# Kernel optimization log

Hardware: AMD Instinct MI355X
Metric: run time of the kernel (lower is better)

Reference implementation:

```python
import jax, jax.numpy as jnp
import numpy as np
import math

EPS = 1e-9
NORM = 1.0 / math.sqrt(20.0)  # num_neighbours=20 default


def _mixing(x1, x2, B, W, b):
    # nn.Bilinear (no bias): x_bi[n,k] = sum_ij x1[n,i] B[k,i,j] x2[n,j]
    x_bi = jnp.einsum('ni,kij->nkj', x1, B)
    x_bi = jnp.einsum('nkj,nj->nk', x_bi, x2)
    x = jnp.concatenate([x1, x2, x_bi], axis=-1)
    return x @ W.T + b


def _rowstd(x):
    # torch.std default: unbiased (ddof=1)
    return jnp.std(x, axis=1, ddof=1, keepdims=True)


def setup_inputs() -> dict:
    key = jax.random.key(0)
    N, E = 100000, 2000000
    DN, DE, DA_N, DA_E = 32, 32, 3, 1
    ks = jax.random.split(key, 24)

    def nrm(k, shape, fan_in):
        return jax.random.normal(k, shape, dtype=jnp.float32) / np.sqrt(fan_in)

    inp = {
        'xn': jax.random.normal(ks[0], (N, DN), dtype=jnp.float32),
        'xn_attr': jax.random.normal(ks[1], (N, DA_N), dtype=jnp.float32),
        'xe_attr': jax.random.normal(ks[2], (E, DA_E), dtype=jnp.float32),
        'xe_src': jax.random.randint(ks[3], (E,), 0, N),
        'xe_dst': jax.random.randint(ks[4], (E,), 0, N),
        # fc1: Linear(1, xe_dim); fc2: Linear(1, xn_dim)
        'W_fc1': nrm(ks[5], (DE, 1), 1), 'b_fc1': jnp.zeros((DE,), jnp.float32),
        'W_fc2': nrm(ks[6], (DN, 1), 1), 'b_fc2': jnp.zeros((DN,), jnp.float32),
        # mix_xn: Mixing(DN, DA_N, DN)
        'B_mix_xn': nrm(ks[7], (DN, DN, DA_N), DN * DA_N),
        'W_mix_xn': nrm(ks[8], (DN, 2 * DN + DA_N), 2 * DN + DA_N),
        'b_mix_xn': jnp.zeros((DN,), jnp.float32),
        # nodes_to_edges.mix: Mixing(DN, DN, DN)
        'B_n2e': nrm(ks[9], (DN, DN, DN), DN * DN),
        'W_n2e': nrm(ks[10], (DN, 3 * DN), 3 * DN),
        'b_n2e': jnp.zeros((DN,), jnp.float32),
        # mix_xe: Mixing(DE, DA_E, DE)
        'B_mix_xe': nrm(ks[11], (DE, DE, DA_E), DE * DA_E),
        'W_mix_xe': nrm(ks[12], (DE, 2 * DE + DA_E), 2 * DE + DA_E),
        'b_mix_xe': jnp.zeros((DE,), jnp.float32),
        # edges_to_nodes.mix: Mixing(DE, DE, DE)
        'B_e2n': nrm(ks[13], (DE, DE, DE), DE * DE),
        'W_e2n': nrm(ks[14], (DE, 3 * DE), 3 * DE),
        'b_e2n': jnp.zeros((DE,), jnp.float32),
    }
    return inp


def reference(xn, xn_attr, xe_attr, xe_src, xe_dst,
              W_fc1, b_fc1, W_fc2, b_fc2,
              B_mix_xn, W_mix_xn, b_mix_xn,
              B_n2e, W_n2e, b_n2e,
              B_mix_xe, W_mix_xe, b_mix_xe,
              B_e2n, W_e2n, b_e2n):
    n_nodes = xn.shape[0]
    # node mixing + per-row std norm
    xn = _mixing(xn, xn_attr, B_mix_xn, W_mix_xn, b_mix_xn)
    xn = xn / (_rowstd(xn) + EPS)
    # fc1 weight: [E, xe_dim]
    w1 = jax.nn.silu(xe_attr @ W_fc1.T + b_fc1)
    # NodesToEdges: gather -> grad/ave -> mixing
    xg, xd = xn[xe_src], xn[xe_dst]
    xe = _mixing(w1 * (xg - xd), w1 * (xg + xd) * 0.5, B_n2e, W_n2e, b_n2e)
    xe = _mixing(xe, xe_attr, B_mix_xe, W_mix_xe, b_mix_xe)
    xe = xe / (_rowstd(xe) + EPS)
    # fc2 weight: [E, xn_dim]
    w2 = jax.nn.silu(xe_attr @ W_fc2.T + b_fc2)
    # EdgesToNodes: scatter-add over dst/src, diff/sum, mixing
    wxe = w2 * xe
    xn1 = jax.ops.segment_sum(wxe, xe_dst, num_segments=n_nodes) * NORM
    xn2 = jax.ops.segment_sum(wxe, xe_src, num_segments=n_nodes) * NORM
    xn = _mixing(xn1 - xn2, xn1 + xn2, B_e2n, W_e2n, b_e2n)
    xn = jax.nn.silu(xn)
    xn = xn / (_rowstd(xn) + EPS)
    return xn
```

## Files before the change

### kernel.cpp

```cpp
#include <hip/hip_runtime.h>
#include <hip/hip_bf16.h>

#define N_NODES 100000
#define N_EDGES 2000000
#define EPS 1e-9f
#define NORMC 0.22360679774997896f

#define BKSZ   256
#define NBK1   391
#define NBK    782
#define NSB    256
#define CE     7813
#define NITEMS 4000000

typedef short s8 __attribute__((ext_vector_type(8)));
typedef float f4 __attribute__((ext_vector_type(4)));

__device__ __forceinline__ float silu_f(float x) {
    return x / (1.0f + __expf(-x));
}

__device__ __forceinline__ ushort f2bfu(float f) {
    union { __hip_bfloat16 b; ushort u; } cv;
    cv.b = __float2bfloat16(f);
    return cv.u;
}

__device__ __forceinline__ uint pkbf(float lo, float hi) {
    float2 t; t.x = lo; t.y = hi;
    union { __hip_bfloat162 b; uint u; } cv;
    cv.b = __float22bfloat162_rn(t);
    return cv.u;
}


__device__ float mext(const float* __restrict__ W, const float* __restrict__ B,
                      const float* __restrict__ bias, int n, int i, int j) {
    if (i < 32 && j < 32) {
        float r = 0.f;
        #pragma unroll
        for (int m = 0; m < 32; ++m) r += W[n*96 + 64 + m] * B[m*1024 + i*32 + j];
        return r;
    }
    if (i < 32) return W[n*96 + i];
    if (j < 32) return W[n*96 + 32 + j];
    return bias[n];
}

__global__ void prep_kernel(const float* __restrict__ W_n2e, const float* __restrict__ B_n2e,
                            const float* __restrict__ b_n2e,
                            const float* __restrict__ W_e2n, const float* __restrict__ B_e2n,
                            const float* __restrict__ b_e2n,
                            const float* __restrict__ W_mix_xn, const float* __restrict__ B_mix_xn,
                            const float* __restrict__ b_mix_xn,
                            const float* __restrict__ W_mix_xe, const float* __restrict__ B_mix_xe,
                            const float* __restrict__ b_mix_xe,
                            ushort* __restrict__ MF, ushort* __restrict__ MG,
                            float* __restrict__ BpN, float* __restrict__ WxE,
                            float* __restrict__ CtE) {
    int t = blockIdx.x * blockDim.x + threadIdx.x;
    if (t < 69632) {
        int u = (t < 34816) ? t : t - 34816;
        int tt = u & 7, lane = (u >> 3) & 63, rest = u >> 9;
        int nt = rest & 1, kk = rest >> 1;
        int n = nt*16 + (lane & 15);
        int kl = ((lane >> 4) & 3) * 8 + tt;
        int i, j;
        if (kk < 33) { i = kk; j = kl; } else { i = kl; j = 32; }
        if (t < 34816) MF[u] = f2bfu(mext(W_n2e, B_n2e, b_n2e, n, i, j));
        else           MG[u] = f2bfu(mext(W_e2n, B_e2n, b_e2n, n, i, j));
    } else if (t < 73856) {
        int u = t - 69632;
        int k = u & 31, ij = u >> 5;
        int i = ij >> 2, j = ij & 3;
        float r;
        if (i < 32 && j < 3) {
            r = 0.f;
            #pragma unroll
            for (int m = 0; m < 32; ++m) r += W_mix_xn[k*67 + 35 + m] * B_mix_xn[m*96 + i*3 + j];
        } else if (i < 32 && j == 3) {
            r = W_mix_xn[k*67 + i];
        } else if (i == 32 && j < 3) {
            r = W_mix_xn[k*67 + 32 + j];
        } else {
            r = b_mix_xn[k];
        }
        BpN[ij*32 + k] = r;
    } else if (t < 74912) {
        int u = t - 73856;
        int k = u & 31, i = u >> 5;
        WxE[i*32 + k] = (i < 32) ? W_mix_xe[k*65 + i] : b_mix_xe[k];
    } else if (t < 75968) {
        int u = t - 74912;
        int k = u & 31, i = u >> 5;
        float r;
        if (i < 32) {
            r = 0.f;
            #pragma unroll
            for (int m = 0; m < 32; ++m) r += W_mix_xe[k*65 + 33 + m] * B_mix_xe[m*32 + i];
        } else {
            r = W_mix_xe[k*65 + 32];
        }
        CtE[i*32 + k] = r;
    }
}

__global__ void zero_kernel(float4* __restrict__ p, int n4) {
    int i = blockIdx.x * blockDim.x + threadIdx.x;
    int stride = gridDim.x * blockDim.x;
    float4 z = {0.f, 0.f, 0.f, 0.f};
    for (; i < n4; i += stride) p[i] = z;
}

__global__ __launch_bounds__(256) void node_kernel(
    const float* __restrict__ xn, const float* __restrict__ xn_attr,
    const float* __restrict__ BpN, float* __restrict__ xn_norm) {
    int n = blockIdx.x * 256 + threadIdx.x;
    if (n >= N_NODES) return;
    float x[33];
    const float4* xr = (const float4*)(xn + (size_t)n * 32);
    #pragma unroll
    for (int q = 0; q < 8; ++q) {
        float4 v = xr[q];
        x[q*4+0] = v.x; x[q*4+1] = v.y; x[q*4+2] = v.z; x[q*4+3] = v.w;
    }
    x[32] = 1.f;
    float at[4];
    at[0] = xn_attr[n*3]; at[1] = xn_attr[n*3+1]; at[2] = xn_attr[n*3+2]; at[3] = 1.f;

    float acc[32];
    #pragma unroll
    for (int k = 0; k < 32; ++k) acc[k] = 0.f;
    #pragma unroll
    for (int i = 0; i < 33; ++i) {
        #pragma unroll
        for (int j = 0; j < 4; ++j) {
            float s = x[i] * at[j];
            const float* bp = BpN + (i*4 + j) * 32;
            #pragma unroll
            for (int k = 0; k < 32; ++k) acc[k] = fmaf(bp[k], s, acc[k]);
        }
    }
    float mean = 0.f;
    #pragma unroll
    for (int k = 0; k < 32; ++k) mean += acc[k];
    mean *= (1.0f / 32.0f);
    float var = 0.f;
    #pragma unroll
    for (int k = 0; k < 32; ++k) { float d = acc[k] - mean; var += d * d; }
    var *= (1.0f / 31.0f);
    float inv = 1.0f / (sqrtf(var) + EPS);
    float4* out = (float4*)(xn_norm + (size_t)n * 32);
    #pragma unroll
    for (int q = 0; q < 8; ++q) {
        float4 v;
        v.x = acc[q*4+0]*inv; v.y = acc[q*4+1]*inv; v.z = acc[q*4+2]*inv; v.w = acc[q*4+3]*inv;
        out[q] = v;
    }
}


__global__ __launch_bounds__(256) void count_kernel(
    const int* __restrict__ xe_src, const int* __restrict__ xe_dst,
    int* __restrict__ cntg) {
    __shared__ int cnt[NBK];
    int tid = threadIdx.x, b = blockIdx.x;
    for (int k = tid; k < NBK; k += 256) cnt[k] = 0;
    __syncthreads();
    int e0 = b * CE;
    for (int i = tid; i < CE; i += 256) {
        int e = e0 + i;
        if (e < N_EDGES) {
            atomicAdd(&cnt[xe_dst[e] >> 8], 1);
            atomicAdd(&cnt[NBK1 + (xe_src[e] >> 8)], 1);
        }
    }
    __syncthreads();
    for (int k = tid; k < NBK; k += 256) cntg[k * NSB + b] = cnt[k];
}

#define SCAN_TOT (NBK * NSB)

__global__ __launch_bounds__(1024) void scan_kernel(
    const int* __restrict__ cntg, int* __restrict__ scang) {
    __shared__ int part[1024];
    int t = threadIdx.x;
    const int CHUNK = 196;
    int base = t * CHUNK;
    int s = 0;
    for (int i = 0; i < CHUNK; ++i) {
        int idx = base + i;
        if (idx < SCAN_TOT) s += cntg[idx];
    }
    part[t] = s;
    __syncthreads();
    for (int off = 1; off < 1024; off <<= 1) {
        int v = part[t];
        int add = (t >= off) ? part[t - off] : 0;
        __syncthreads();
        part[t] = v + add;
        __syncthreads();
    }
    int run = (t == 0) ? 0 : part[t - 1];
    for (int i = 0; i < CHUNK; ++i) {
        int idx = base + i;
        if (idx < SCAN_TOT) {
            int c = cntg[idx];
            scang[idx] = run;
            run += c;
        }
    }
}

__global__ __launch_bounds__(256) void scatter_kernel(
    const int* __restrict__ xe_src, const int* __restrict__ xe_dst,
    const int* __restrict__ scang, int* __restrict__ bucketed) {
    __shared__ int cur[NBK];
    int tid = threadIdx.x, b = blockIdx.x;
    for (int k = tid; k < NBK; k += 256) cur[k] = scang[k * NSB + b];
    __syncthreads();
    int e0 = b * CE;
    for (int i = tid; i < CE; i += 256) {
        int e = e0 + i;
        if (e < N_EDGES) {
            int d = xe_dst[e];
            int p = atomicAdd(&cur[d >> 8], 1);
            bucketed[p] = e | ((d & 255) << 21);
            int s_ = xe_src[e];
            p = atomicAdd(&cur[NBK1 + (s_ >> 8)], 1);
            bucketed[p] = e | ((s_ & 255) << 21);
        }
    }
}

__global__ __launch_bounds__(256) void gather_kernel(
    const ushort* __restrict__ wxe, const int* __restrict__ bucketed,
    const int* __restrict__ scang, float* __restrict__ sd0) {
    __shared__ float accs[BKSZ * 33];
    int tid = threadIdx.x, bk = blockIdx.x;
    for (int i = tid; i < BKSZ * 33; i += 256) accs[i] = 0.f;
    __syncthreads();
    int start = scang[bk * NSB];
    int end = (bk == NBK - 1) ? NITEMS : scang[(bk + 1) * NSB];
    int q = tid >> 2, g = tid & 3;
    uint4 z4; z4.x = 0u; z4.y = 0u; z4.z = 0u; z4.w = 0u;

    int i0 = start + q;
    int p0 = (i0 < end) ? bucketed[i0] : 0;
    int p1 = (i0 + 64 < end) ? bucketed[i0 + 64] : 0;
    uint4 r0 = (i0 < end)
             ? *(const uint4*)(wxe + (size_t)(p0 & 0x1FFFFF) * 32 + g * 8) : z4;

    for (int i = i0; i < end; i += 64) {
        int pn = (i + 128 < end) ? bucketed[i + 128] : 0;
        uint4 r1 = (i + 64 < end)
                 ? *(const uint4*)(wxe + (size_t)(p1 & 0x1FFFFF) * 32 + g * 8) : z4;
        int ln = (p0 >> 21) & 255;
        float* ap = &accs[ln * 33 + g * 8];
        uint uu[4] = {r0.x, r0.y, r0.z, r0.w};
        #pragma unroll
        for (int c = 0; c < 4; ++c) {
            uint u = uu[c];
            atomicAdd(&ap[c*2],     __uint_as_float((u & 0xFFFFu) << 16));
            atomicAdd(&ap[c*2 + 1], __uint_as_float(u & 0xFFFF0000u));
        }
        p0 = p1; p1 = pn; r0 = r1;
    }
    __syncthreads();
    int side = (bk < NBK1) ? 0 : 1;
    int nb = side ? bk - NBK1 : bk;
    float* out = sd0 + (size_t)side * 3211264 + (size_t)nb * BKSZ * 32;
    for (int i = tid; i < BKSZ * 32; i += 256) {
        int node = i >> 5, k = i & 31;
        out[i] = accs[node * 33 + k];
    }
}


__device__ __forceinline__ void gemm33(const ushort* __restrict__ sM,
                                       float* __restrict__ a_f,
                                       const ushort* __restrict__ ab,
                                       const float* __restrict__ biasv, int tid) {
    int lane = tid & 63, wv = tid >> 6;
    int m = lane & 15, h = lane >> 4;
    int base = wv * 64;
    float bfv[4][8];
    s8 araw[4];
    #pragma unroll
    for (int g = 0; g < 4; ++g) {
        const ushort* rp = &ab[(size_t)(base + g*16 + m) * 72];
        union { s8 v; ushort s[8]; } braw;
        braw.v = *(const s8*)&rp[h*8];
        #pragma unroll
        for (int t = 0; t < 8; ++t) {
            union { uint u; float f; } cv; cv.u = ((uint)braw.s[t]) << 16;
            bfv[g][t] = cv.f;
        }
        araw[g] = *(const s8*)&rp[32 + h*8];
    }
    f4 c[4][2];
    #pragma unroll
    for (int g = 0; g < 4; ++g) {
        c[g][0] = (f4){0.f, 0.f, 0.f, 0.f};
        c[g][1] = (f4){0.f, 0.f, 0.f, 0.f};
    }
    const s8* M8 = (const s8*)sM;
    #pragma unroll
    for (int kk = 0; kk < 33; ++kk) {
        s8 mf0 = M8[(kk*2 + 0)*64 + lane];
        s8 mf1 = M8[(kk*2 + 1)*64 + lane];
        #pragma unroll
        for (int g = 0; g < 4; ++g) {
            float as = a_f[(size_t)(base + g*16 + m) * 33 + kk];
            union { s8 v; uint u[4]; } af;
            #pragma unroll
            for (int t = 0; t < 4; ++t) af.u[t] = pkbf(as * bfv[g][2*t], as * bfv[g][2*t+1]);
            c[g][0] = __builtin_amdgcn_mfma_f32_16x16x32_bf16(af.v, mf0, c[g][0], 0, 0, 0);
            c[g][1] = __builtin_amdgcn_mfma_f32_16x16x32_bf16(af.v, mf1, c[g][1], 0, 0, 0);
        }
    }
    {
        s8 mf0 = M8[66*64 + lane];
        s8 mf1 = M8[67*64 + lane];
        #pragma unroll
        for (int g = 0; g < 4; ++g) {
            c[g][0] = __builtin_amdgcn_mfma_f32_16x16x32_bf16(araw[g], mf0, c[g][0], 0, 0, 0);
            c[g][1] = __builtin_amdgcn_mfma_f32_16x16x32_bf16(araw[g], mf1, c[g][1], 0, 0, 0);
        }
    }
    float b0 = biasv[m], b1 = biasv[16 + m];
    #pragma unroll
    for (int g = 0; g < 4; ++g) {
        int rowb = base + g*16 + h*4;
        #pragma unroll
        for (int r = 0; r < 4; ++r) {
            a_f[(size_t)(rowb + r) * 33 + m]      = c[g][0][r] + b0;
            a_f[(size_t)(rowb + r) * 33 + 16 + m] = c[g][1][r] + b1;
        }
    }
}

#define TILES_E 7813

template<bool STORE>
__global__ __launch_bounds__(256, 1) void edge_kernel(
    const float* __restrict__ xn_norm, const float* __restrict__ xe_attr,
    const int* __restrict__ xe_src, const int* __restrict__ xe_dst,
    const float* __restrict__ W_fc1, const float* __restrict__ b_fc1,
    const float* __restrict__ W_fc2, const float* __restrict__ b_fc2,
    const ushort* __restrict__ MF, const float* __restrict__ biasE,
    const float* __restrict__ WxE, const float* __restrict__ CtE,
    float* __restrict__ acc1, float* __restrict__ acc2,
    ushort* __restrict__ wxe) {
    __shared__ __align__(16) ushort sM[34816];
    __shared__ __align__(16) float  a_f[256 * 33];
    __shared__ __align__(16) ushort ab[256 * 72];
    int tid = threadIdx.x;
    {
        const float4* s4p = (const float4*)MF;
        float4* d4p = (float4*)sM;
        #pragma unroll
        for (int i = 0; i < 17; ++i) d4p[tid + i*256] = s4p[tid + i*256];
    }
    uint* ab32 = (uint*)ab;

    int t = blockIdx.x;
    float attrP = 0.f; int srcP = 0, dstP = 0; bool okP = false;
    float4 gP[8], dP[8];
    {
        int e = t*256 + tid;
        okP = e < N_EDGES;
        int ec = okP ? e : 0;
        attrP = xe_attr[ec]; srcP = xe_src[ec]; dstP = xe_dst[ec];
        const float4* gp = (const float4*)(xn_norm + (size_t)srcP * 32);
        const float4* dp = (const float4*)(xn_norm + (size_t)dstP * 32);
        #pragma unroll
        for (int q = 0; q < 8; ++q) { gP[q] = gp[q]; dP[q] = dp[q]; }
    }

    for (; t < TILES_E; t += 256) {
        float attr = attrP; int csrc = srcP, cdst = dstP; bool okC = okP;
        float vs = okC ? 1.f : 0.f;
        #pragma unroll
        for (int q = 0; q < 8; ++q) {
            float4 g = gP[q], d = dP[q];
            float gg[4] = {g.x, g.y, g.z, g.w};
            float dd[4] = {d.x, d.y, d.z, d.w};
            #pragma unroll
            for (int p = 0; p < 2; ++p) {
                int k = q*4 + p*2;
                float w0 = silu_f(attr * W_fc1[k]   + b_fc1[k])   * vs;
                float w1 = silu_f(attr * W_fc1[k+1] + b_fc1[k+1]) * vs;
                float av0 = w0 * (gg[2*p]   - dd[2*p]);
                float av1 = w1 * (gg[2*p+1] - dd[2*p+1]);
                float bv0 = w0 * (gg[2*p]   + dd[2*p])   * 0.5f;
                float bv1 = w1 * (gg[2*p+1] + dd[2*p+1]) * 0.5f;
                a_f[tid*33 + k]   = av0;
                a_f[tid*33 + k+1] = av1;
                ab32[tid*36 + (k>>1)]      = pkbf(bv0, bv1);
                ab32[tid*36 + 16 + (k>>1)] = pkbf(av0, av1);
            }
        }
        a_f[tid*33 + 32] = 1.f;

        int tn = t + 256;
        if (tn < TILES_E) {
            int e = tn*256 + tid;
            okP = e < N_EDGES;
            int ec = okP ? e : 0;
            attrP = xe_attr[ec]; srcP = xe_src[ec]; dstP = xe_dst[ec];
            const float4* gp = (const float4*)(xn_norm + (size_t)srcP * 32);
            const float4* dp = (const float4*)(xn_norm + (size_t)dstP * 32);
            #pragma unroll
            for (int q = 0; q < 8; ++q) { gP[q] = gp[q]; dP[q] = dp[q]; }
        }
        __syncthreads();

        gemm33(sM, a_f, ab, biasE, tid);
        __syncthreads();

        float2 y2[16];
        #pragma unroll
        for (int k2 = 0; k2 < 16; ++k2) y2[k2] = make_float2(0.f, 0.f);
        for (int i = 0; i < 33; ++i) {
            float xi = a_f[tid*33 + i];
            const float2* wx2 = (const float2*)(WxE + i * 32);
            const float2* ct2 = (const float2*)(CtE + i * 32);
            #pragma unroll
            for (int k2 = 0; k2 < 16; ++k2) {
                float2 w = wx2[k2], ctv = ct2[k2];
                float lx = fmaf(attr, ctv.x, w.x);
                float ly = fmaf(attr, ctv.y, w.y);
                y2[k2].x = fmaf(lx, xi, y2[k2].x);
                y2[k2].y = fmaf(ly, xi, y2[k2].y);
            }
        }
        float mean = 0.f;
        #pragma unroll
        for (int k2 = 0; k2 < 16; ++k2) mean += y2[k2].x + y2[k2].y;
        mean *= (1.0f / 32.0f);
        float var = 0.f;
        #pragma unroll
        for (int k2 = 0; k2 < 16; ++k2) {
            float dx = y2[k2].x - mean, dy = y2[k2].y - mean;
            var += dx*dx + dy*dy;
        }
        var *= (1.0f / 31.0f);
        float inv = 1.0f / (sqrtf(var) + EPS);

        if (okC) {
            if (STORE) {
                uint pkv[16];
                #pragma unroll
                for (int k2 = 0; k2 < 16; ++k2) {
                    float w20 = silu_f(attr * W_fc2[2*k2]   + b_fc2[2*k2]);
                    float w21 = silu_f(attr * W_fc2[2*k2+1] + b_fc2[2*k2+1]);
                    pkv[k2] = pkbf(w20 * y2[k2].x * inv, w21 * y2[k2].y * inv);
                }
                uint4* wp = (uint4*)(wxe + (size_t)(t*256 + tid) * 32);
                #pragma unroll
                for (int q = 0; q < 4; ++q) {
                    uint4 v; v.x = pkv[q*4]; v.y = pkv[q*4+1]; v.z = pkv[q*4+2]; v.w = pkv[q*4+3];
                    wp[q] = v;
                }
            } else {
                float* p1 = acc1 + (size_t)cdst * 32;
                float* p2 = acc2 + (size_t)csrc * 32;
                #pragma unroll
                for (int k = 0; k < 32; ++k) {
                    float yk = (k & 1) ? y2[k>>1].y : y2[k>>1].x;
                    float w2 = silu_f(attr * W_fc2[k] + b_fc2[k]);
                    float v = w2 * yk * inv;
                    unsafeAtomicAdd(p1 + k, v);
                    unsafeAtomicAdd(p2 + k, v);
                }
            }
        }
    }
}

#define TILES_F 391

__global__ __launch_bounds__(256, 1) void final_kernel(
    const float* __restrict__ acc1, const float* __restrict__ acc2,
    const ushort* __restrict__ MG, const float* __restrict__ biasG,
    float* __restrict__ out) {
    __shared__ __align__(16) ushort sM[34816];
    __shared__ __align__(16) float  a_f[256 * 33];
    __shared__ __align__(16) ushort ab[256 * 72];
    int tid = threadIdx.x;
    {
        const float4* s4p = (const float4*)MG;
        float4* d4p = (float4*)sM;
        #pragma unroll
        for (int i = 0; i < 17; ++i) d4p[tid + i*256] = s4p[tid + i*256];
    }
    uint* ab32 = (uint*)ab;

    for (int t = blockIdx.x; t < TILES_F; t += 256) {
        int n = t*256 + tid;
        bool ok = n < N_NODES;
        int nn = ok ? n : 0;
        float vs = ok ? 1.f : 0.f;
        const float4* p1 = (const float4*)(acc1 + (size_t)nn * 32);
        const float4* p2 = (const float4*)(acc2 + (size_t)nn * 32);
        #pragma unroll
        for (int q = 0; q < 8; ++q) {
            float4 u1 = p1[q], u2 = p2[q];
            float a1[4] = {u1.x, u1.y, u1.z, u1.w};
            float a2[4] = {u2.x, u2.y, u2.z, u2.w};
            #pragma unroll
            for (int p = 0; p < 2; ++p) {
                int k = q*4 + p*2;
                float dv0 = (a1[2*p]   - a2[2*p])   * NORMC * vs;
                float dv1 = (a1[2*p+1] - a2[2*p+1]) * NORMC * vs;
                float sv0 = (a1[2*p]   + a2[2*p])   * NORMC * vs;
                float sv1 = (a1[2*p+1] + a2[2*p+1]) * NORMC * vs;
                a_f[tid*33 + k]   = dv0;
                a_f[tid*33 + k+1] = dv1;
                ab32[tid*36 + (k>>1)]      = pkbf(sv0, sv1);
                ab32[tid*36 + 16 + (k>>1)] = pkbf(dv0, dv1);
            }
        }
        a_f[tid*33 + 32] = 1.f;
        __syncthreads();

        gemm33(sM, a_f, ab, biasG, tid);
        __syncthreads();

        if (ok) {
            float z[32];
            float mean = 0.f;
            #pragma unroll
            for (int k = 0; k < 32; ++k) { z[k] = silu_f(a_f[tid*33 + k]); mean += z[k]; }
            mean *= (1.0f / 32.0f);
            float var = 0.f;
            #pragma unroll
            for (int k = 0; k < 32; ++k) { float d = z[k] - mean; var += d * d; }
            var *= (1.0f / 31.0f);
            float inv = 1.0f / (sqrtf(var) + EPS);
            float4* op = (float4*)(out + (size_t)n * 32);
            #pragma unroll
            for (int q = 0; q < 8; ++q) {
                float4 v;
                v.x = z[q*4+0]*inv; v.y = z[q*4+1]*inv; v.z = z[q*4+2]*inv; v.w = z[q*4+3]*inv;
                op[q] = v;
            }
        }
    }
}

extern "C" void kernel_launch(void* const* d_in, const int* in_sizes, int n_in,
                              void* d_out, int out_size, void* d_ws, size_t ws_size,
                              hipStream_t stream) {
    const float* xn       = (const float*)d_in[0];
    const float* xn_attr  = (const float*)d_in[1];
    const float* xe_attr  = (const float*)d_in[2];
    const int*   xe_src   = (const int*)d_in[3];
    const int*   xe_dst   = (const int*)d_in[4];
    const float* W_fc1    = (const float*)d_in[5];
    const float* b_fc1    = (const float*)d_in[6];
    const float* W_fc2    = (const float*)d_in[7];
    const float* b_fc2    = (const float*)d_in[8];
    const float* B_mix_xn = (const float*)d_in[9];
    const float* W_mix_xn = (const float*)d_in[10];
    const float* b_mix_xn = (const float*)d_in[11];
    const float* B_n2e    = (const float*)d_in[12];
    const float* W_n2e    = (const float*)d_in[13];
    const float* b_n2e    = (const float*)d_in[14];
    const float* B_mix_xe = (const float*)d_in[15];
    const float* W_mix_xe = (const float*)d_in[16];
    const float* b_mix_xe = (const float*)d_in[17];
    const float* B_e2n    = (const float*)d_in[18];
    const float* W_e2n    = (const float*)d_in[19];
    const float* b_e2n    = (const float*)d_in[20];

    float* ws = (float*)d_ws;
    const size_t MAIN_BYTES = 46065088ULL * 4ULL;
    bool big = ws_size >= MAIN_BYTES;

    if (big) {
        float*  xn_norm = ws;
        float*  sd0     = ws + 3200000;
        float*  sd1     = ws + 6411264;
        ushort* MF      = (ushort*)(ws + 9622528);
        ushort* MG      = MF + 34816;
        float*  BpN     = ws + 9657344;
        float*  WxE     = ws + 9661568;
        float*  CtE     = ws + 9662624;
        ushort* wxe     = (ushort*)(ws + 9663680);
        int*    bucketed= (int*)(ws + 41663680);
        int*    cntg    = (int*)(ws + 45663680);
        int*    scang   = (int*)(ws + 45864384);

        prep_kernel<<<297, 256, 0, stream>>>(W_n2e, B_n2e, b_n2e, W_e2n, B_e2n, b_e2n,
                                             W_mix_xn, B_mix_xn, b_mix_xn,
                                             W_mix_xe, B_mix_xe, b_mix_xe,
                                             MF, MG, BpN, WxE, CtE);
        node_kernel<<<391, 256, 0, stream>>>(xn, xn_attr, BpN, xn_norm);
        count_kernel<<<NSB, 256, 0, stream>>>(xe_src, xe_dst, cntg);
        scan_kernel<<<1, 1024, 0, stream>>>(cntg, scang);
        scatter_kernel<<<NSB, 256, 0, stream>>>(xe_src, xe_dst, scang, bucketed);
        edge_kernel<true><<<256, 256, 0, stream>>>(xn_norm, xe_attr, xe_src, xe_dst,
                                                   W_fc1, b_fc1, W_fc2, b_fc2,
                                                   MF, b_n2e, WxE, CtE,
                                                   nullptr, nullptr, wxe);
        gather_kernel<<<NBK, 256, 0, stream>>>(wxe, bucketed, scang, sd0);
        final_kernel<<<391, 256, 0, stream>>>(sd0, sd1, MG, b_e2n, (float*)d_out);
    } else {
        float*  xn_norm = ws;
        float*  acc1    = ws + 3200000;
        float*  acc2    = ws + 6400000;
        ushort* MF      = (ushort*)(ws + 9600000);
        ushort* MG      = MF + 34816;
        float*  BpN     = ws + 9600000 + 34816;
        float*  WxE     = BpN + 4224;
        float*  CtE     = WxE + 1056;

        prep_kernel<<<297, 256, 0, stream>>>(W_n2e, B_n2e, b_n2e, W_e2n, B_e2n, b_e2n,
                                             W_mix_xn, B_mix_xn, b_mix_xn,
                                             W_mix_xe, B_mix_xe, b_mix_xe,
                                             MF, MG, BpN, WxE, CtE);
        zero_kernel<<<2048, 256, 0, stream>>>((float4*)acc1, 1600000);
        node_kernel<<<391, 256, 0, stream>>>(xn, xn_attr, BpN, xn_norm);
        edge_kernel<false><<<256, 256, 0, stream>>>(xn_norm, xe_attr, xe_src, xe_dst,
                                                    W_fc1, b_fc1, W_fc2, b_fc2,
                                                    MF, b_n2e, WxE, CtE,
                                                    acc1, acc2, nullptr);
        final_kernel<<<391, 256, 0, stream>>>(acc1, acc2, MG, b_e2n, (float*)d_out);
    }
}
```

Before: 2.013 ms.

## Store edge outputs in src-bucket order and split gather into src/dst passes

The edge kernel now writes each edge's weighted message directly to its position in the source-sorted order, using a position array built during scatter. The src-side gather then reads contiguously with a byte lane index, and the dst-side gather indexes through a packed (position, lane) array. The gemm staging buffer is shrunk by recomputing the bf16 copy of the first operand from the float tile instead of storing it twice. This trades scattered reads in the gather for scattered writes in the edge kernel and adds an extra per-edge index load.

```diff
diff --git a/kernel.cpp b/kernel.cpp
--- a/kernel.cpp
+++ b/kernel.cpp
@@ -11,10 +11,13 @@
 #define NBK    782
 #define NSB    256
 #define CE     7813
-#define NITEMS 4000000
+#define SCAN_TOT (NBK * NSB)
+#define TILES_E 7813
+#define TILES_F 391
 
 typedef short s8 __attribute__((ext_vector_type(8)));
 typedef float f4 __attribute__((ext_vector_type(4)));
+typedef uint  u4 __attribute__((ext_vector_type(4)));
 
 __device__ __forceinline__ float silu_f(float x) {
     return x / (1.0f + __expf(-x));
@@ -179,10 +182,7 @@
     for (int k = tid; k < NBK; k += 256) cntg[k * NSB + b] = cnt[k];
 }
 
-#define SCAN_TOT (NBK * NSB)
-
-__global__ __launch_bounds__(1024) void scan_kernel(
-    const int* __restrict__ cntg, int* __restrict__ scang) {
+__global__ __launch_bounds__(1024) void scan_kernel(int* __restrict__ cntg) {
     __shared__ int part[1024];
     int t = threadIdx.x;
     const int CHUNK = 196;
@@ -206,7 +206,7 @@
         int idx = base + i;
         if (idx < SCAN_TOT) {
             int c = cntg[idx];
-            scang[idx] = run;
+            cntg[idx] = run;
             run += c;
         }
     }
@@ -214,7 +214,8 @@
 
 __global__ __launch_bounds__(256) void scatter_kernel(
     const int* __restrict__ xe_src, const int* __restrict__ xe_dst,
-    const int* __restrict__ scang, int* __restrict__ bucketed) {
+    const int* __restrict__ scang, int* __restrict__ poss,
+    unsigned char* __restrict__ srcln, int* __restrict__ bucketed_dst) {
     __shared__ int cur[NBK];
     int tid = threadIdx.x, b = blockIdx.x;
     for (int k = tid; k < NBK; k += 256) cur[k] = scang[k * NSB + b];
@@ -223,39 +224,77 @@
     for (int i = tid; i < CE; i += 256) {
         int e = e0 + i;
         if (e < N_EDGES) {
+            int s_ = xe_src[e];
+            int p2 = atomicAdd(&cur[NBK1 + (s_ >> 8)], 1) - N_EDGES;
+            poss[e] = p2;
+            srcln[p2] = (unsigned char)(s_ & 255);
             int d = xe_dst[e];
-            int p = atomicAdd(&cur[d >> 8], 1);
-            bucketed[p] = e | ((d & 255) << 21);
-            int s_ = xe_src[e];
-            p = atomicAdd(&cur[NBK1 + (s_ >> 8)], 1);
-            bucketed[p] = e | ((s_ & 255) << 21);
-        }
-    }
-}
-
-__global__ __launch_bounds__(256) void gather_kernel(
-    const ushort* __restrict__ wxe, const int* __restrict__ bucketed,
+            int pd = atomicAdd(&cur[d >> 8], 1);
+            bucketed_dst[pd] = (p2 << 8) | (d & 255);
+        }
+    }
+}
+
+__global__ __launch_bounds__(256) void gather_src(
+    const ushort* __restrict__ wxe2, const unsigned char* __restrict__ srcln,
+    const int* __restrict__ scang, float* __restrict__ sd1) {
+    __shared__ float accs[BKSZ * 33];
+    int tid = threadIdx.x, bk = blockIdx.x;
+    for (int i = tid; i < BKSZ * 33; i += 256) accs[i] = 0.f;
+    __syncthreads();
+    int start = scang[(NBK1 + bk) * NSB] - N_EDGES;
+    int end = (bk == NBK1 - 1) ? N_EDGES : scang[(NBK1 + bk + 1) * NSB] - N_EDGES;
+    int q = tid >> 2, g = tid & 3;
+    uint4 z4; z4.x = 0u; z4.y = 0u; z4.z = 0u; z4.w = 0u;
+
+    int i0 = start + q;
+    int ln0 = (i0 < end) ? (int)srcln[i0] : 0;
+    uint4 r0 = (i0 < end) ? *(const uint4*)(wxe2 + (size_t)i0 * 32 + g * 8) : z4;
+    for (int i = i0; i < end; i += 64) {
+        int in = i + 64;
+        int ln1 = (in < end) ? (int)srcln[in] : 0;
+        uint4 r1 = (in < end) ? *(const uint4*)(wxe2 + (size_t)in * 32 + g * 8) : z4;
+        float* ap = &accs[ln0 * 33 + g * 8];
+        uint uu[4] = {r0.x, r0.y, r0.z, r0.w};
+        #pragma unroll
+        for (int c = 0; c < 4; ++c) {
+            uint u = uu[c];
+            atomicAdd(&ap[c*2],     __uint_as_float((u & 0xFFFFu) << 16));
+            atomicAdd(&ap[c*2 + 1], __uint_as_float(u & 0xFFFF0000u));
+        }
+        ln0 = ln1; r0 = r1;
+    }
+    __syncthreads();
+    float* out = sd1 + (size_t)bk * BKSZ * 32;
+    for (int i2 = tid; i2 < BKSZ * 32; i2 += 256) {
+        int node = i2 >> 5, k = i2 & 31;
+        out[i2] = accs[node * 33 + k];
+    }
+}
+
+__global__ __launch_bounds__(256) void gather_dst(
+    const ushort* __restrict__ wxe2, const int* __restrict__ bucketed_dst,
     const int* __restrict__ scang, float* __restrict__ sd0) {
     __shared__ float accs[BKSZ * 33];
     int tid = threadIdx.x, bk = blockIdx.x;
     for (int i = tid; i < BKSZ * 33; i += 256) accs[i] = 0.f;
     __syncthreads();
     int start = scang[bk * NSB];
-    int end = (bk == NBK - 1) ? NITEMS : scang[(bk + 1) * NSB];
+    int end = (bk == NBK1 - 1) ? N_EDGES : scang[(bk + 1) * NSB];
     int q = tid >> 2, g = tid & 3;
     uint4 z4; z4.x = 0u; z4.y = 0u; z4.z = 0u; z4.w = 0u;
 
     int i0 = start + q;
-    int p0 = (i0 < end) ? bucketed[i0] : 0;
-    int p1 = (i0 + 64 < end) ? bucketed[i0 + 64] : 0;
+    int p0 = (i0 < end) ? bucketed_dst[i0] : 0;
+    int p1 = (i0 + 64 < end) ? bucketed_dst[i0 + 64] : 0;
     uint4 r0 = (i0 < end)
-             ? *(const uint4*)(wxe + (size_t)(p0 & 0x1FFFFF) * 32 + g * 8) : z4;
+             ? *(const uint4*)(wxe2 + (size_t)(p0 >> 8) * 32 + g * 8) : z4;
 
     for (int i = i0; i < end; i += 64) {
-        int pn = (i + 128 < end) ? bucketed[i + 128] : 0;
+        int pn = (i + 128 < end) ? bucketed_dst[i + 128] : 0;
         uint4 r1 = (i + 64 < end)
-                 ? *(const uint4*)(wxe + (size_t)(p1 & 0x1FFFFF) * 32 + g * 8) : z4;
-        int ln = (p0 >> 21) & 255;
+                 ? *(const uint4*)(wxe2 + (size_t)(p1 >> 8) * 32 + g * 8) : z4;
+        int ln = p0 & 255;
         float* ap = &accs[ln * 33 + g * 8];
         uint uu[4] = {r0.x, r0.y, r0.z, r0.w};
         #pragma unroll
@@ -267,15 +306,12 @@
         p0 = p1; p1 = pn; r0 = r1;
     }
     __syncthreads();
-    int side = (bk < NBK1) ? 0 : 1;
-    int nb = side ? bk - NBK1 : bk;
-    float* out = sd0 + (size_t)side * 3211264 + (size_t)nb * BKSZ * 32;
-    for (int i = tid; i < BKSZ * 32; i += 256) {
-        int node = i >> 5, k = i & 31;
-        out[i] = accs[node * 33 + k];
-    }
-}
-
+    float* out = sd0 + (size_t)bk * BKSZ * 32;
+    for (int i2 = tid; i2 < BKSZ * 32; i2 += 256) {
+        int node = i2 >> 5, k = i2 & 31;
+        out[i2] = accs[node * 33 + k];
+    }
+}
 
 __device__ __forceinline__ void gemm33(const ushort* __restrict__ sM,
                                        float* __restrict__ a_f,
@@ -285,18 +321,15 @@
     int m = lane & 15, h = lane >> 4;
     int base = wv * 64;
     float bfv[4][8];
-    s8 araw[4];
     #pragma unroll
     for (int g = 0; g < 4; ++g) {
-        const ushort* rp = &ab[(size_t)(base + g*16 + m) * 72];
         union { s8 v; ushort s[8]; } braw;
-        braw.v = *(const s8*)&rp[h*8];
+        braw.v = *(const s8*)&ab[(size_t)(base + g*16 + m) * 40 + h*8];
         #pragma unroll
         for (int t = 0; t < 8; ++t) {
             union { uint u; float f; } cv; cv.u = ((uint)braw.s[t]) << 16;
             bfv[g][t] = cv.f;
         }
-        araw[g] = *(const s8*)&rp[32 + h*8];
     }
     f4 c[4][2];
     #pragma unroll
@@ -324,8 +357,12 @@
         s8 mf1 = M8[67*64 + lane];
         #pragma unroll
         for (int g = 0; g < 4; ++g) {
-            c[g][0] = __builtin_amdgcn_mfma_f32_16x16x32_bf16(araw[g], mf0, c[g][0], 0, 0, 0);
-            c[g][1] = __builtin_amdgcn_mfma_f32_16x16x32_bf16(araw[g], mf1, c[g][1], 0, 0, 0);
+            const float* arow = &a_f[(size_t)(base + g*16 + m) * 33 + h*8];
+            union { s8 v; uint u[4]; } af;
+            #pragma unroll
+            for (int t = 0; t < 4; ++t) af.u[t] = pkbf(arow[2*t], arow[2*t+1]);
+            c[g][0] = __builtin_amdgcn_mfma_f32_16x16x32_bf16(af.v, mf0, c[g][0], 0, 0, 0);
+            c[g][1] = __builtin_amdgcn_mfma_f32_16x16x32_bf16(af.v, mf1, c[g][1], 0, 0, 0);
         }
     }
     float b0 = biasv[m], b1 = biasv[16 + m];
@@ -340,9 +377,41 @@
     }
 }
 
-#define TILES_E 7813
-
-template<bool STORE>
+__device__ __forceinline__ float mixe_std(const float* __restrict__ a_f, int tid,
+                                          float attr,
+                                          const float* __restrict__ WxE,
+                                          const float* __restrict__ CtE,
+                                          float2* __restrict__ y2) {
+    #pragma unroll
+    for (int k2 = 0; k2 < 16; ++k2) y2[k2] = make_float2(0.f, 0.f);
+    for (int i = 0; i < 33; ++i) {
+        float xi = a_f[tid*33 + i];
+        const float2* wx2 = (const float2*)(WxE + i * 32);
+        const float2* ct2 = (const float2*)(CtE + i * 32);
+        #pragma unroll
+        for (int k2 = 0; k2 < 16; ++k2) {
+            float2 w = wx2[k2], ctv = ct2[k2];
+            float lx = fmaf(attr, ctv.x, w.x);
+            float ly = fmaf(attr, ctv.y, w.y);
+            y2[k2].x = fmaf(lx, xi, y2[k2].x);
+            y2[k2].y = fmaf(ly, xi, y2[k2].y);
+        }
+    }
+    float mean = 0.f;
+    #pragma unroll
+    for (int k2 = 0; k2 < 16; ++k2) mean += y2[k2].x + y2[k2].y;
+    mean *= (1.0f / 32.0f);
+    float var = 0.f;
+    #pragma unroll
+    for (int k2 = 0; k2 < 16; ++k2) {
+        float dx = y2[k2].x - mean, dy = y2[k2].y - mean;
+        var += dx*dx + dy*dy;
+    }
+    var *= (1.0f / 31.0f);
+    return 1.0f / (sqrtf(var) + EPS);
+}
+
+template<int MODE>
 __global__ __launch_bounds__(256, 1) void edge_kernel(
     const float* __restrict__ xn_norm, const float* __restrict__ xe_attr,
     const int* __restrict__ xe_src, const int* __restrict__ xe_dst,
@@ -351,10 +420,10 @@
     const ushort* __restrict__ MF, const float* __restrict__ biasE,
     const float* __restrict__ WxE, const float* __restrict__ CtE,
     float* __restrict__ acc1, float* __restrict__ acc2,
-    ushort* __restrict__ wxe) {
+    ushort* __restrict__ wxe2, const int* __restrict__ poss) {
     __shared__ __align__(16) ushort sM[34816];
     __shared__ __align__(16) float  a_f[256 * 33];
-    __shared__ __align__(16) ushort ab[256 * 72];
+    __shared__ __align__(16) ushort ab[256 * 40];
     int tid = threadIdx.x;
     {
         const float4* s4p = (const float4*)MF;
@@ -365,13 +434,14 @@
     uint* ab32 = (uint*)ab;
 
     int t = blockIdx.x;
-    float attrP = 0.f; int srcP = 0, dstP = 0; bool okP = false;
+    float attrP = 0.f; int srcP = 0, dstP = 0, posP = 0; bool okP = false;
     float4 gP[8], dP[8];
     {
         int e = t*256 + tid;
         okP = e < N_EDGES;
         int ec = okP ? e : 0;
         attrP = xe_attr[ec]; srcP = xe_src[ec]; dstP = xe_dst[ec];
+        if (MODE == 1) posP = poss[ec];
         const float4* gp = (const float4*)(xn_norm + (size_t)srcP * 32);
         const float4* dp = (const float4*)(xn_norm + (size_t)dstP * 32);
         #pragma unroll
@@ -379,7 +449,8 @@
     }
 
     for (; t < TILES_E; t += 256) {
-        float attr = attrP; int csrc = srcP, cdst = dstP; bool okC = okP;
+        float attr = attrP; int csrc = srcP, cdst = dstP, cpos = posP;
+        bool okC = okP;
         float vs = okC ? 1.f : 0.f;
         #pragma unroll
         for (int q = 0; q < 8; ++q) {
@@ -397,8 +468,7 @@
                 float bv1 = w1 * (gg[2*p+1] + dd[2*p+1]) * 0.5f;
                 a_f[tid*33 + k]   = av0;
                 a_f[tid*33 + k+1] = av1;
-                ab32[tid*36 + (k>>1)]      = pkbf(bv0, bv1);
-                ab32[tid*36 + 16 + (k>>1)] = pkbf(av0, av1);
+                ab32[tid*20 + (k>>1)] = pkbf(bv0, bv1);
             }
         }
         a_f[tid*33 + 32] = 1.f;
@@ -409,6 +479,7 @@
             okP = e < N_EDGES;
             int ec = okP ? e : 0;
             attrP = xe_attr[ec]; srcP = xe_src[ec]; dstP = xe_dst[ec];
+            if (MODE == 1) posP = poss[ec];
             const float4* gp = (const float4*)(xn_norm + (size_t)srcP * 32);
             const float4* dp = (const float4*)(xn_norm + (size_t)dstP * 32);
             #pragma unroll
@@ -420,36 +491,10 @@
         __syncthreads();
 
         float2 y2[16];
-        #pragma unroll
-        for (int k2 = 0; k2 < 16; ++k2) y2[k2] = make_float2(0.f, 0.f);
-        for (int i = 0; i < 33; ++i) {
-            float xi = a_f[tid*33 + i];
-            const float2* wx2 = (const float2*)(WxE + i * 32);
-            const float2* ct2 = (const float2*)(CtE + i * 32);
-            #pragma unroll
-            for (int k2 = 0; k2 < 16; ++k2) {
-                float2 w = wx2[k2], ctv = ct2[k2];
-                float lx = fmaf(attr, ctv.x, w.x);
-                float ly = fmaf(attr, ctv.y, w.y);
-                y2[k2].x = fmaf(lx, xi, y2[k2].x);
-                y2[k2].y = fmaf(ly, xi, y2[k2].y);
-            }
-        }
-        float mean = 0.f;
-        #pragma unroll
-        for (int k2 = 0; k2 < 16; ++k2) mean += y2[k2].x + y2[k2].y;
-        mean *= (1.0f / 32.0f);
-        float var = 0.f;
-        #pragma unroll
-        for (int k2 = 0; k2 < 16; ++k2) {
-            float dx = y2[k2].x - mean, dy = y2[k2].y - mean;
-            var += dx*dx + dy*dy;
-        }
-        var *= (1.0f / 31.0f);
-        float inv = 1.0f / (sqrtf(var) + EPS);
+        float inv = mixe_std(a_f, tid, attr, WxE, CtE, y2);
 
         if (okC) {
-            if (STORE) {
+            if (MODE == 1) {
                 uint pkv[16];
                 #pragma unroll
                 for (int k2 = 0; k2 < 16; ++k2) {
@@ -457,11 +502,11 @@
                     float w21 = silu_f(attr * W_fc2[2*k2+1] + b_fc2[2*k2+1]);
                     pkv[k2] = pkbf(w20 * y2[k2].x * inv, w21 * y2[k2].y * inv);
                 }
-                uint4* wp = (uint4*)(wxe + (size_t)(t*256 + tid) * 32);
+                u4* wp = (u4*)(wxe2 + (size_t)cpos * 32);
                 #pragma unroll
                 for (int q = 0; q < 4; ++q) {
-                    uint4 v; v.x = pkv[q*4]; v.y = pkv[q*4+1]; v.z = pkv[q*4+2]; v.w = pkv[q*4+3];
-                    wp[q] = v;
+                    u4 v = (u4){pkv[q*4], pkv[q*4+1], pkv[q*4+2], pkv[q*4+3]};
+                    __builtin_nontemporal_store(v, wp + q);
                 }
             } else {
                 float* p1 = acc1 + (size_t)cdst * 32;
@@ -470,16 +515,14 @@
                 for (int k = 0; k < 32; ++k) {
                     float yk = (k & 1) ? y2[k>>1].y : y2[k>>1].x;
                     float w2 = silu_f(attr * W_fc2[k] + b_fc2[k]);
-                    float v = w2 * yk * inv;
-                    unsafeAtomicAdd(p1 + k, v);
-                    unsafeAtomicAdd(p2 + k, v);
+                    float vv = w2 * yk * inv;
+                    unsafeAtomicAdd(p1 + k, vv);
+                    unsafeAtomicAdd(p2 + k, vv);
                 }
             }
         }
     }
 }
-
-#define TILES_F 391
 
 __global__ __launch_bounds__(256, 1) void final_kernel(
     const float* __restrict__ acc1, const float* __restrict__ acc2,
@@ -487,7 +530,7 @@
     float* __restrict__ out) {
     __shared__ __align__(16) ushort sM[34816];
     __shared__ __align__(16) float  a_f[256 * 33];
-    __shared__ __align__(16) ushort ab[256 * 72];
+    __shared__ __align__(16) ushort ab[256 * 40];
     int tid = threadIdx.x;
     {
         const float4* s4p = (const float4*)MG;
@@ -518,8 +561,7 @@
                 float sv1 = (a1[2*p+1] + a2[2*p+1]) * NORMC * vs;
                 a_f[tid*33 + k]   = dv0;
                 a_f[tid*33 + k+1] = dv1;
-                ab32[tid*36 + (k>>1)]      = pkbf(sv0, sv1);
-                ab32[tid*36 + 16 + (k>>1)] = pkbf(dv0, dv1);
+                ab32[tid*20 + (k>>1)] = pkbf(sv0, sv1);
             }
         }
         a_f[tid*33 + 32] = 1.f;
@@ -576,22 +618,22 @@
     const float* b_e2n    = (const float*)d_in[20];
 
     float* ws = (float*)d_ws;
-    const size_t MAIN_BYTES = 46065088ULL * 4ULL;
-    bool big = ws_size >= MAIN_BYTES;
-
-    if (big) {
+    const size_t T1_BYTES = 46347488ULL * 4ULL;
+
+    if (ws_size >= T1_BYTES) {
         float*  xn_norm = ws;
         float*  sd0     = ws + 3200000;
-        float*  sd1     = ws + 6411264;
-        ushort* MF      = (ushort*)(ws + 9622528);
-        ushort* MG      = MF + 34816;
-        float*  BpN     = ws + 9657344;
-        float*  WxE     = ws + 9661568;
-        float*  CtE     = ws + 9662624;
-        ushort* wxe     = (ushort*)(ws + 9663680);
-        int*    bucketed= (int*)(ws + 41663680);
-        int*    cntg    = (int*)(ws + 45663680);
-        int*    scang   = (int*)(ws + 45864384);
+        float*  sd1     = ws + 6403072;
+        ushort* MF      = (ushort*)(ws + 9606144);
+        ushort* MG      = (ushort*)(ws + 9623552);
+        float*  BpN     = ws + 9640960;
+        float*  WxE     = ws + 9645184;
+        float*  CtE     = ws + 9646240;
+        ushort* wxe2    = (ushort*)(ws + 9647296);
+        int*    poss    = (int*)(ws + 41647296);
+        unsigned char* srcln = (unsigned char*)(ws + 43647296);
+        int*    bucketed_dst = (int*)(ws + 44147296);
+        int*    cntg    = (int*)(ws + 46147296);
 
         prep_kernel<<<297, 256, 0, stream>>>(W_n2e, B_n2e, b_n2e, W_e2n, B_e2n, b_e2n,
                                              W_mix_xn, B_mix_xn, b_mix_xn,
@@ -599,13 +641,15 @@
                                              MF, MG, BpN, WxE, CtE);
         node_kernel<<<391, 256, 0, stream>>>(xn, xn_attr, BpN, xn_norm);
         count_kernel<<<NSB, 256, 0, stream>>>(xe_src, xe_dst, cntg);
-        scan_kernel<<<1, 1024, 0, stream>>>(cntg, scang);
-        scatter_kernel<<<NSB, 256, 0, stream>>>(xe_src, xe_dst, scang, bucketed);
-        edge_kernel<true><<<256, 256, 0, stream>>>(xn_norm, xe_attr, xe_src, xe_dst,
-                                                   W_fc1, b_fc1, W_fc2, b_fc2,
-                                                   MF, b_n2e, WxE, CtE,
-                                                   nullptr, nullptr, wxe);
-        gather_kernel<<<NBK, 256, 0, stream>>>(wxe, bucketed, scang, sd0);
+        scan_kernel<<<1, 1024, 0, stream>>>(cntg);
+        scatter_kernel<<<NSB, 256, 0, stream>>>(xe_src, xe_dst, cntg,
+                                                poss, srcln, bucketed_dst);
+        edge_kernel<1><<<256, 256, 0, stream>>>(xn_norm, xe_attr, xe_src, xe_dst,
+                                                W_fc1, b_fc1, W_fc2, b_fc2,
+                                                MF, b_n2e, WxE, CtE,
+                                                nullptr, nullptr, wxe2, poss);
+        gather_src<<<NBK1, 256, 0, stream>>>(wxe2, srcln, cntg, sd1);
+        gather_dst<<<NBK1, 256, 0, stream>>>(wxe2, bucketed_dst, cntg, sd0);
         final_kernel<<<391, 256, 0, stream>>>(sd0, sd1, MG, b_e2n, (float*)d_out);
     } else {
         float*  xn_norm = ws;
@@ -623,10 +667,10 @@
                                              MF, MG, BpN, WxE, CtE);
         zero_kernel<<<2048, 256, 0, stream>>>((float4*)acc1, 1600000);
         node_kernel<<<391, 256, 0, stream>>>(xn, xn_attr, BpN, xn_norm);
-        edge_kernel<false><<<256, 256, 0, stream>>>(xn_norm, xe_attr, xe_src, xe_dst,
-                                                    W_fc1, b_fc1, W_fc2, b_fc2,
-                                                    MF, b_n2e, WxE, CtE,
-                                                    acc1, acc2, nullptr);
+        edge_kernel<0><<<256, 256, 0, stream>>>(xn_norm, xe_attr, xe_src, xe_dst,
+                                                W_fc1, b_fc1, W_fc2, b_fc2,
+                                                MF, b_n2e, WxE, CtE,
+                                                acc1, acc2, nullptr, nullptr);
         final_kernel<<<391, 256, 0, stream>>>(acc1, acc2, MG, b_e2n, (float*)d_out);
     }
 }
```

Result: slower. 2.056 ms (+2.2%).
